# Kernel tuning notes

Measured on AMD Instinct MI355X. Metric: run time of the kernel, lower is better.

## Reference

```python
import jax, jax.numpy as jnp
import numpy as np

H = 9
N1, N2, N3 = 100000, 25000, 6250
E1, E2, E3 = 1200000, 300000, 75000
LAYERS = {"l1": (6, 32), "l2": (32, 64), "l3": (64, 128), "l4": (128, 128),
          "r1": (128, 64), "r2": (128, 64), "r3": (64, 32), "r4": (64, 32)}


def setup_inputs() -> dict:
    key = jax.random.key(0)
    ks = iter(jax.random.split(key, 64))
    d = {}
    d["x"] = jax.random.normal(next(ks), (N1, 6), jnp.float32)
    d["ei1"] = jax.random.randint(next(ks), (2, E1), 0, N1)
    d["ei2"] = jax.random.randint(next(ks), (2, E2), 0, N2)
    d["ei3"] = jax.random.randint(next(ks), (2, E3), 0, N3)
    d["clust2"] = jax.random.randint(next(ks), (N1,), 0, N2)
    d["clust3"] = jax.random.randint(next(ks), (N2,), 0, N3)
    for name, (cin, cout) in LAYERS.items():
        d[name + "_u"] = jax.random.normal(next(ks), (cin, H), jnp.float32) * 0.1
        d[name + "_c"] = jax.random.normal(next(ks), (H,), jnp.float32) * 0.1
        d[name + "_w"] = jax.random.normal(next(ks), (cin, H * cout), jnp.float32) * (1.0 / np.sqrt(cin))
        d[name + "_b"] = jnp.zeros((cout,), jnp.float32)
    d["fc1_w"] = jax.random.normal(next(ks), (32, 1024), jnp.float32) * (1.0 / np.sqrt(32))
    d["fc1_b"] = jnp.zeros((1024,), jnp.float32)
    d["fc2_w"] = jax.random.normal(next(ks), (1024, 3), jnp.float32) * (1.0 / np.sqrt(1024))
    d["fc2_b"] = jnp.zeros((3,), jnp.float32)
    return d


def _feast(x, ei, u, c, W, b):
    """FeaStConv (Verma et al., PyG semantics): per-edge head attention
    q = softmax(u^T (x_j - x_i) + c), mean aggregation, self-loops added."""
    n = x.shape[0]
    out = W.shape[1] // H
    loop = jnp.arange(n)
    src = jnp.concatenate([ei[0], loop])  # message source j
    dst = jnp.concatenate([ei[1], loop])  # message target i
    q = jax.nn.softmax((x[src] - x[dst]) @ u + c, axis=1)  # [E, H]
    msg = jnp.zeros((src.shape[0], out), x.dtype)
    for h in range(H):  # fixed head loop keeps peak memory at [E, out]
        msg = msg + q[:, h:h + 1] * (x @ W[:, h * out:(h + 1) * out])[src]
    agg = jax.ops.segment_sum(msg, dst, num_segments=n)
    cnt = jax.ops.segment_sum(jnp.ones((dst.shape[0],), x.dtype), dst, num_segments=n)
    return agg / cnt[:, None] + b  # cnt >= 1 thanks to self-loops


def _pool_mean(x, clust, n_out):
    s = jax.ops.segment_sum(x, clust, num_segments=n_out)
    c = jax.ops.segment_sum(jnp.ones((x.shape[0],), x.dtype), clust, num_segments=n_out)
    return s / jnp.maximum(c, 1.0)[:, None]


def _lrelu(v):
    return jax.nn.leaky_relu(v, 0.1)


def reference(x, ei1, ei2, ei3, clust2, clust3,
              l1_u, l1_c, l1_w, l1_b, l2_u, l2_c, l2_w, l2_b,
              l3_u, l3_c, l3_w, l3_b, l4_u, l4_c, l4_w, l4_b,
              r1_u, r1_c, r1_w, r1_b, r2_u, r2_c, r2_w, r2_b,
              r3_u, r3_c, r3_w, r3_b, r4_u, r4_c, r4_w, r4_b,
              fc1_w, fc1_b, fc2_w, fc2_b):
    x1 = _lrelu(_feast(x, ei1, l1_u, l1_c, l1_w, l1_b))           # [N1, 32]
    x2 = _pool_mean(x1, clust2, N2)                                # [N2, 32]
    x2 = _lrelu(_feast(x2, ei2, l2_u, l2_c, l2_w, l2_b))           # [N2, 64]
    x3 = _pool_mean(x2, clust3, N3)                                # [N3, 64]
    x3 = _lrelu(_feast(x3, ei3, l3_u, l3_c, l3_w, l3_b))           # [N3, 128]
    x3 = _lrelu(_feast(x3, ei3, l4_u, l4_c, l4_w, l4_b))           # [N3, 128]
    f2 = _feast(x3[clust3], ei2, r1_u, r1_c, r1_w, r1_b)           # unpool -> [N2, 64] (no act)
    x2 = jnp.concatenate([x2, f2], axis=1)                         # [N2, 128]
    x2 = _lrelu(_feast(x2, ei2, r2_u, r2_c, r2_w, r2_b))           # [N2, 64]
    f1 = _feast(x2[clust2], ei1, r3_u, r3_c, r3_w, r3_b)           # unpool -> [N1, 32] (no act)
    x1 = jnp.concatenate([x1, f1], axis=1)                         # [N1, 64]
    y = _lrelu(_feast(x1, ei1, r4_u, r4_c, r4_w, r4_b))            # [N1, 32]
    y = _lrelu(y @ fc1_w + fc1_b)                                  # [N1, 1024]
    y = y @ fc2_w + fc2_b                                          # [N1, 3]
    return y / jnp.maximum(jnp.linalg.norm(y, axis=1, keepdims=True), 1e-12)
```

## Files before the change

kernel.cpp:

```cpp
#include <hip/hip_runtime.h>
#include <cstddef>
#include <cstdint>

#define NH 9
#define QLD 16

typedef _Float16 f16x8 __attribute__((ext_vector_type(8)));
typedef _Float16 f16x4 __attribute__((ext_vector_type(4)));
typedef _Float16 f16x2 __attribute__((ext_vector_type(2)));
typedef float f32x4 __attribute__((ext_vector_type(4)));

static const int cN1 = 100000, cN2 = 25000, cN3 = 6250;
static const int cE1 = 1200000, cE2 = 300000, cE3 = 75000;

static inline unsigned ceil_div(size_t a, size_t b) { return (unsigned)((a + b - 1) / b); }

struct PackArgs {
    const float* W[8];
    const float* c[8];
    const float* u[8];
    int K[8], OUT[8], Kpad[8], base[8];
    int total;
};

__global__ void pack_b_all(PackArgs a, _Float16* __restrict__ wt)
{
    int i = blockIdx.x * 256 + threadIdx.x;
    if (i >= a.total) return;
    int li = 0;
#pragma unroll
    for (int j = 1; j < 8; ++j) li += (i >= a.base[j]);
    int r = i - a.base[li];
    int Kp = a.Kpad[li], K = a.K[li], OUT = a.OUT[li];
    int NC = NH * OUT, NCO = NC + OUT;
    int n = r / Kp, k = r % Kp;
    float v = 0.f;
    if (k < K) {
        if (n < NC) v = a.W[li][(size_t)k * NC + n];
        else if (n < NCO) {
            const float* cv = a.c[li];
            float t[NH], m = -1e30f;
#pragma unroll
            for (int h = 0; h < NH; ++h) { t[h] = cv[h]; m = fmaxf(m, t[h]); }
            float den = 0.f;
#pragma unroll
            for (int h = 0; h < NH; ++h) { t[h] = __expf(t[h] - m); den += t[h]; }
            int o = n - NC;
            float acc = 0.f;
#pragma unroll
            for (int h = 0; h < NH; ++h) acc += t[h] * a.W[li][(size_t)k * NC + h * OUT + o];
            v = acc / den;
        } else {
            v = a.u[li][(size_t)k * NH + (n - NCO)];
        }
    }
    wt[i] = (_Float16)v;
}

template <typename AT>
__global__ __launch_bounds__(256) void gemm_merged(
    const AT* __restrict__ A, int lda, const int* __restrict__ ridx,
    const _Float16* __restrict__ WT, int kpad,
    _Float16* __restrict__ C, _Float16* __restrict__ xuh,
    int M, int K, int NC, int OUT)
{
    const int N = NC + OUT + NH;
    const int NCO = NC + OUT;
    const int ldc = NCO + 16;
    const int BM = 64, BK = 32, LK = 40;
    __shared__ _Float16 As[BM][LK];
    __shared__ _Float16 Bs[64][LK];
    const int tid = threadIdx.x;
    const int row0 = blockIdx.y * BM, col0 = blockIdx.x * 64;
    const int lane = tid & 63, wv = tid >> 6;
    const int g = lane >> 4, r16 = lane & 15;
    const int wr = wv >> 1, wc = wv & 1;
    f32x4 acc[2][2] = {};
    for (int k0 = 0; k0 < K; k0 += BK) {
        if constexpr (sizeof(AT) == 2) {
            int r = tid >> 2, c0 = (tid & 3) * 8;
            int gr = row0 + r, gk = k0 + c0;
            f16x8 h = {};
            if (gr < M) {
                int ar = ridx ? ridx[gr] : gr;
                h = *(const f16x8*)((const _Float16*)A + (size_t)ar * lda + gk);
            }
            *(f16x8*)&As[r][c0] = h;
        } else {
            for (int l = tid; l < 512; l += 256) {
                int r = l >> 3, c0 = (l & 7) * 4;
                int gr = row0 + r, gk = k0 + c0;
                float v0 = 0.f, v1 = 0.f, v2 = 0.f, v3 = 0.f;
                if (gr < M) {
                    int ar = ridx ? ridx[gr] : gr;
                    const float* ap = (const float*)A + (size_t)ar * lda + gk;
                    if (gk < K)     v0 = ap[0];
                    if (gk + 1 < K) v1 = ap[1];
                    if (gk + 2 < K) v2 = ap[2];
                    if (gk + 3 < K) v3 = ap[3];
                }
                f16x4 h;
                h[0] = (_Float16)v0; h[1] = (_Float16)v1; h[2] = (_Float16)v2; h[3] = (_Float16)v3;
                *(f16x4*)&As[r][c0] = h;
            }
        }
        {
            int nn = tid >> 2, c0 = (tid & 3) * 8;
            int gn = col0 + nn, gk = k0 + c0;
            f16x8 h = {};
            if (gn < N) h = *(const f16x8*)(WT + (size_t)gn * kpad + gk);
            *(f16x8*)&Bs[nn][c0] = h;
        }
        __syncthreads();
        f16x8 af[2], bf[2];
#pragma unroll
        for (int i = 0; i < 2; ++i) af[i] = *(const f16x8*)&As[wr * 32 + i * 16 + r16][g * 8];
#pragma unroll
        for (int j = 0; j < 2; ++j) bf[j] = *(const f16x8*)&Bs[wc * 32 + j * 16 + r16][g * 8];
#pragma unroll
        for (int i = 0; i < 2; ++i)
#pragma unroll
            for (int j = 0; j < 2; ++j)
                acc[i][j] = __builtin_amdgcn_mfma_f32_16x16x32_f16(af[i], bf[j], acc[i][j], 0, 0, 0);
        __syncthreads();
    }
#pragma unroll
    for (int i = 0; i < 2; ++i)
#pragma unroll
        for (int j = 0; j < 2; ++j) {
            int gc = col0 + wc * 32 + j * 16 + r16;
            if (gc >= N) continue;
            int tcol = gc - NCO;
#pragma unroll
            for (int rr = 0; rr < 4; ++rr) {
                int gr = row0 + wr * 32 + i * 16 + g * 4 + rr;
                if (gr >= M) continue;
                _Float16 val = (_Float16)acc[i][j][rr];
                C[(size_t)gr * ldc + gc] = val;
                if (tcol >= 0) xuh[(size_t)gr * QLD + tcol] = val;
            }
        }
}

__global__ void count_idx(const int* __restrict__ idx, int n, int* __restrict__ cnt)
{
    int i = blockIdx.x * 256 + threadIdx.x;
    if (i < n) atomicAdd(&cnt[idx[i]], 1);
}

__global__ void count_both(const int* __restrict__ src, const int* __restrict__ dst, int E,
                           int* __restrict__ scnt, int* __restrict__ dcnt)
{
    int i = blockIdx.x * 256 + threadIdx.x;
    if (i >= E) return;
    atomicAdd(&scnt[src[i]], 1);
    atomicAdd(&dcnt[dst[i]], 1);
}

__global__ __launch_bounds__(1024) void scan1(const int* __restrict__ in, int* __restrict__ out,
                                              int* __restrict__ part, int n)
{
    __shared__ int wsum[16];
    const int tid = threadIdx.x, lane = tid & 63, wv = tid >> 6;
    int i = blockIdx.x * 1024 + tid;
    int v = (i < n) ? in[i] : 0;
    int acc = v;
#pragma unroll
    for (int off = 1; off < 64; off <<= 1) {
        int t = __shfl_up(acc, off);
        if (lane >= off) acc += t;
    }
    if (lane == 63) wsum[wv] = acc;
    __syncthreads();
    if (wv == 0 && lane < 16) {
        int s = wsum[lane];
        int a2 = s;
#pragma unroll
        for (int off = 1; off < 16; off <<= 1) {
            int t = __shfl_up(a2, off);
            if (lane >= off) a2 += t;
        }
        wsum[lane] = a2 - s;
    }
    __syncthreads();
    int ex = wsum[wv] + acc - v;
    if (i < n) out[i] = ex;
    if (part && tid == 1023) part[blockIdx.x] = ex + v;
}

__global__ void scan_add(int* __restrict__ out, const int* __restrict__ part, int n)
{
    int i = blockIdx.x * 1024 + threadIdx.x;
    if (i < n) out[i] += part[blockIdx.x];
}

__global__ void fill_src(const int* __restrict__ soffB, const int* __restrict__ scnt,
                         int* __restrict__ srcs, int n, int ebias)
{
    int i = blockIdx.x * 256 + threadIdx.x;
    if (i >= n) return;
    int b = soffB[i] - ebias, c = scnt[i];
    for (int k = 0; k < c; ++k) srcs[b + k] = i;
}

__global__ void scatter_dst(const int* __restrict__ src, const int* __restrict__ dst, int E,
                            const int* __restrict__ soffB, int* __restrict__ curs,
                            int* __restrict__ dsts, int ebias)
{
    int e = blockIdx.x * 256 + threadIdx.x;
    if (e >= E) return;
    int s = src[e];
    int ps = soffB[s] - ebias + atomicAdd(&curs[s], 1);
    dsts[ps] = dst[e];
}

template <int OUT>
__global__ __launch_bounds__(256) void feast_msg(
    const int* __restrict__ srcs, const int* __restrict__ dsts, int E,
    const _Float16* __restrict__ xwa, const _Float16* __restrict__ xuh,
    const float* __restrict__ cvec, const int* __restrict__ ds,
    int* __restrict__ curd, _Float16* __restrict__ msg)
{
    constexpr int NC = NH * OUT, NCO = NC + OUT, LDR = NCO + 16;
    const int T = OUT / 32;
    size_t tid = (size_t)blockIdx.x * 256 + threadIdx.x;
    int e = (int)(tid / T);
    int ch = (int)(tid % T);
    if (e >= E) return;
    int s = srcs[e], d = dsts[e];
    int beg = ds[d];
    int deg = ds[d + 1] - beg;
    int pd;
    if (T == 1) {
        pd = beg + (atomicAdd(&curd[d], 1) % deg);
    } else {
        int lane = threadIdx.x & 63;
        int pv = 0;
        if (ch == 0) pv = beg + (atomicAdd(&curd[d], 1) % deg);
        pd = __shfl(pv, (lane / T) * T);
    }
    f16x8 u8s = *(const f16x8*)(xwa + (size_t)s * LDR + NCO);
    f16x2 u2s = *(const f16x2*)(xwa + (size_t)s * LDR + NCO + 8);
    f16x8 u8d = *(const f16x8*)(xuh + (size_t)d * QLD);
    f16x2 u2d = *(const f16x2*)(xuh + (size_t)d * QLD + 8);
    float t[NH];
    float m = -1e30f;
#pragma unroll
    for (int h = 0; h < 8; ++h) {
        t[h] = (float)u8s[h] - (float)u8d[h] + cvec[h];
        m = fmaxf(m, t[h]);
    }
    t[8] = (float)u2s[0] - (float)u2d[0] + cvec[8];
    m = fmaxf(m, t[8]);
    float den = 0.f;
#pragma unroll
    for (int h = 0; h < NH; ++h) { t[h] = __expf(t[h] - m); den += t[h]; }
    float sc = 1.f / (den * (float)(deg + 1));

    const f16x8* xrow = (const f16x8*)(xwa + (size_t)s * LDR);
    float acc[32] = {};
#pragma unroll
    for (int h = 0; h < NH; ++h) {
        float qh = t[h] * sc;
        const f16x8* xh = xrow + h * (OUT / 8) + ch * 4;
#pragma unroll
        for (int v = 0; v < 4; ++v) {
            f16x8 x8 = xh[v];
#pragma unroll
            for (int j = 0; j < 8; ++j) acc[v * 8 + j] += qh * (float)x8[j];
        }
    }
    f16x8* mo = (f16x8*)(msg + (size_t)pd * OUT + ch * 32);
#pragma unroll
    for (int v = 0; v < 4; ++v) {
        f16x8 r;
#pragma unroll
        for (int j = 0; j < 8; ++j) r[j] = (_Float16)acc[v * 8 + j];
        mo[v] = r;
    }
}

template <int OUT>
__global__ __launch_bounds__(256) void feast_red(
    const int* __restrict__ ds,
    const _Float16* __restrict__ msg, const _Float16* __restrict__ xwa,
    const float* __restrict__ bias, _Float16* __restrict__ outp,
    int n, int ldo, int col0, int act,
    const int* __restrict__ clust, float* __restrict__ pooled)
{
    constexpr int NC = NH * OUT, LDR = NC + OUT + 16;
    const int L = OUT / 8;
    size_t tid = (size_t)blockIdx.x * 256 + threadIdx.x;
    int d = (int)(tid / L);
    int p = (int)(tid % L);
    if (d >= n) return;
    int beg = ds[d];
    int end = ds[d + 1];
    int deg = end - beg;
    float acc[8] = {};
    int i = beg;
    for (; i + 2 <= end; i += 2) {
        f16x8 v0 = *(const f16x8*)(msg + (size_t)i * OUT + p * 8);
        f16x8 v1 = *(const f16x8*)(msg + (size_t)(i + 1) * OUT + p * 8);
#pragma unroll
        for (int j = 0; j < 8; ++j) acc[j] += (float)v0[j] + (float)v1[j];
    }
    if (i < end) {
        f16x8 v0 = *(const f16x8*)(msg + (size_t)i * OUT + p * 8);
#pragma unroll
        for (int j = 0; j < 8; ++j) acc[j] += (float)v0[j];
    }
    float sc = 1.f / (float)(deg + 1);
    f16x8 sv = *(const f16x8*)(xwa + (size_t)d * LDR + NC + p * 8);
    float o[8];
    f16x8 oh;
#pragma unroll
    for (int j = 0; j < 8; ++j) {
        float v = acc[j] + (float)sv[j] * sc + bias[p * 8 + j];
        if (act) v = v > 0.f ? v : 0.1f * v;
        o[j] = v;
        oh[j] = (_Float16)v;
    }
    *(f16x8*)(outp + (size_t)d * ldo + col0 + p * 8) = oh;
    if (clust) {
        float* pp = pooled + (size_t)clust[d] * OUT + p * 8;
#pragma unroll
        for (int j = 0; j < 8; ++j) unsafeAtomicAdd(&pp[j], o[j]);
    }
}

__global__ void pool_div(float* __restrict__ pooled, const int* __restrict__ pcnt, int C, int m)
{
    size_t tid = (size_t)blockIdx.x * 256 + threadIdx.x;
    int j = (int)(tid / C);
    if (j >= m) return;
    pooled[tid] /= fmaxf((float)pcnt[j], 1.f);
}

__global__ void w1_to_f16t(const float* __restrict__ w1, _Float16* __restrict__ w1t)
{
    int i = blockIdx.x * 256 + threadIdx.x;
    if (i >= 32 * 1024) return;
    int n = i >> 5, k = i & 31;
    w1t[i] = (_Float16)w1[k * 1024 + n];
}

__global__ __launch_bounds__(256) void fc_head2(
    const _Float16* __restrict__ yin, const _Float16* __restrict__ w1t,
    const float* __restrict__ b1, const float* __restrict__ w2,
    const float* __restrict__ b2, float* __restrict__ outp, int n)
{
    const int lane = threadIdx.x & 63, wv = threadIdx.x >> 6;
    const int g = lane >> 4, r16 = lane & 15;
    const int node0 = blockIdx.x * 64 + wv * 16;

    f16x8 afrag = {};
    int anode = node0 + r16;
    if (anode < n) afrag = *(const f16x8*)(yin + (size_t)anode * 32 + g * 8);

    float o0[4] = {0.f, 0.f, 0.f, 0.f};
    float o1[4] = {0.f, 0.f, 0.f, 0.f};
    float o2[4] = {0.f, 0.f, 0.f, 0.f};
    const f32x4 zero4 = {0.f, 0.f, 0.f, 0.f};

#pragma unroll 2
    for (int t = 0; t < 64; ++t) {
        const f16x8 bfrag = *(const f16x8*)(w1t + ((size_t)(t * 16 + r16)) * 32 + g * 8);
        f32x4 d = __builtin_amdgcn_mfma_f32_16x16x32_f16(afrag, bfrag, zero4, 0, 0, 0);
        int kh = t * 16 + r16;
        float b1v = b1[kh];
        float w20 = w2[kh * 3], w21 = w2[kh * 3 + 1], w22 = w2[kh * 3 + 2];
#pragma unroll
        for (int r = 0; r < 4; ++r) {
            float h = d[r] + b1v;
            h = h > 0.f ? h : 0.1f * h;
            o0[r] += h * w20;
            o1[r] += h * w21;
            o2[r] += h * w22;
        }
    }
#pragma unroll
    for (int r = 0; r < 4; ++r) {
#pragma unroll
        for (int off = 1; off < 16; off <<= 1) {
            o0[r] += __shfl_xor(o0[r], off);
            o1[r] += __shfl_xor(o1[r], off);
            o2[r] += __shfl_xor(o2[r], off);
        }
    }
    if (r16 == 0) {
#pragma unroll
        for (int r = 0; r < 4; ++r) {
            int node = node0 + g * 4 + r;
            if (node >= n) continue;
            float v0 = o0[r] + b2[0];
            float v1 = o1[r] + b2[1];
            float v2 = o2[r] + b2[2];
            float nr = fmaxf(sqrtf(v0 * v0 + v1 * v1 + v2 * v2), 1e-12f);
            outp[(size_t)node * 3 + 0] = v0 / nr;
            outp[(size_t)node * 3 + 1] = v1 / nr;
            outp[(size_t)node * 3 + 2] = v2 / nr;
        }
    }
}

static void launch_msg(int outC, const int* srcs, const int* dsts, int E,
                       const _Float16* xwa, const _Float16* xuh, const float* cvec,
                       const int* ds, int* curd, _Float16* msg, hipStream_t stream)
{
    dim3 g(ceil_div((size_t)E * (outC / 32), 256));
    if (outC == 32)       feast_msg<32><<<g, 256, 0, stream>>>(srcs, dsts, E, xwa, xuh, cvec, ds, curd, msg);
    else if (outC == 64)  feast_msg<64><<<g, 256, 0, stream>>>(srcs, dsts, E, xwa, xuh, cvec, ds, curd, msg);
    else                  feast_msg<128><<<g, 256, 0, stream>>>(srcs, dsts, E, xwa, xuh, cvec, ds, curd, msg);
}

static void launch_red(int outC, const int* ds,
                       const _Float16* msg, const _Float16* xwa, const float* bias,
                       _Float16* outp, int n, int ldo, int col0, int act,
                       const int* clust, float* pooled, hipStream_t stream)
{
    dim3 g(ceil_div((size_t)n * (outC / 8), 256));
    if (outC == 32)       feast_red<32><<<g, 256, 0, stream>>>(ds, msg, xwa, bias, outp, n, ldo, col0, act, clust, pooled);
    else if (outC == 64)  feast_red<64><<<g, 256, 0, stream>>>(ds, msg, xwa, bias, outp, n, ldo, col0, act, clust, pooled);
    else                  feast_red<128><<<g, 256, 0, stream>>>(ds, msg, xwa, bias, outp, n, ldo, col0, act, clust, pooled);
}

extern "C" void kernel_launch(void* const* d_in, const int* in_sizes, int n_in,
                              void* d_out, int out_size, void* d_ws, size_t ws_size,
                              hipStream_t stream)
{
    const float* x      = (const float*)d_in[0];
    const int*   ei1    = (const int*)d_in[1];
    const int*   ei2    = (const int*)d_in[2];
    const int*   ei3    = (const int*)d_in[3];
    const int*   clust2 = (const int*)d_in[4];
    const int*   clust3 = (const int*)d_in[5];
    const float* lp[8][4];
    for (int i = 0; i < 8; ++i)
        for (int j = 0; j < 4; ++j)
            lp[i][j] = (const float*)d_in[6 + i * 4 + j];
    const float* fc1_w = (const float*)d_in[38];
    const float* fc1_b = (const float*)d_in[39];
    const float* fc2_w = (const float*)d_in[40];
    const float* fc2_b = (const float*)d_in[41];
    float* out = (float*)d_out;

    static const int lK[8]   = {6, 32, 64, 128, 128, 128, 64, 64};
    static const int lOUT[8] = {32, 64, 128, 128, 64, 64, 32, 32};

    char* ws = (char*)d_ws;
    size_t off = 0;
    auto alloc = [&](size_t b) { size_t p = off; off += (b + 255) & ~(size_t)255; return p; };
    _Float16* XWA = (_Float16*)(ws + alloc((size_t)cN1 * 336 * 2));
    _Float16* MSG = (_Float16*)(ws + alloc((size_t)cE1 * 32 * 2));
    _Float16* XUH = (_Float16*)(ws + alloc((size_t)cN1 * QLD * 2));
    _Float16* X1CAT = (_Float16*)(ws + alloc((size_t)cN1 * 64 * 2));
    _Float16* X2CAT = (_Float16*)(ws + alloc((size_t)cN2 * 128 * 2));
    _Float16* X2B   = (_Float16*)(ws + alloc((size_t)cN2 * 64 * 2));
    _Float16* X3    = (_Float16*)(ws + alloc((size_t)cN3 * 128 * 2));
    _Float16* YB    = (_Float16*)(ws + alloc((size_t)cN1 * 32 * 2));
    float* GATH = (float*)(ws + alloc((size_t)cN2 * 32 * 4));
    float* P3   = (float*)(ws + alloc((size_t)cN3 * 64 * 4));
    int* SRCS1 = (int*)(ws + alloc((size_t)cE1 * 4));
    int* SRCS2 = (int*)(ws + alloc((size_t)cE2 * 4));
    int* SRCS3 = (int*)(ws + alloc((size_t)cE3 * 4));
    int* DSTS1 = (int*)(ws + alloc((size_t)cE1 * 4));
    int* DSTS2 = (int*)(ws + alloc((size_t)cE2 * 4));
    int* DSTS3 = (int*)(ws + alloc((size_t)cE3 * 4));
    int* DS1 = (int*)(ws + alloc((size_t)2 * cN1 * 4));
    int* DS2 = (int*)(ws + alloc((size_t)2 * cN2 * 4));
    int* DS3 = (int*)(ws + alloc((size_t)2 * cN3 * 4));
    size_t zn = (size_t)4 * (cN1 + cN2 + cN3) + cN2 + cN3;
    int* ZBLK = (int*)(ws + alloc(zn * 4));
    int* CB1 = ZBLK;
    int* CURS1 = CB1 + 2 * cN1;
    int* CURD1 = CURS1 + cN1;
    int* CB2 = CURD1 + cN1;
    int* CURS2 = CB2 + 2 * cN2;
    int* CURD2 = CURS2 + cN2;
    int* CB3 = CURD2 + cN2;
    int* CURS3 = CB3 + 2 * cN3;
    int* CURD3 = CURS3 + cN3;
    int* PC2 = CURD3 + cN3;
    int* PC3 = PC2 + cN2;
    int* PART = (int*)(ws + alloc(1024 * 4));
    _Float16* W1T = (_Float16*)(ws + alloc((size_t)32 * 1024 * 2));
    PackArgs pa;
    int ptot = 0;
    for (int i = 0; i < 8; ++i) {
        pa.W[i] = lp[i][2]; pa.c[i] = lp[i][1]; pa.u[i] = lp[i][0];
        pa.K[i] = lK[i]; pa.OUT[i] = lOUT[i];
        pa.Kpad[i] = (lK[i] + 31) & ~31;
        pa.base[i] = ptot;
        ptot += (NH * lOUT[i] + lOUT[i] + NH) * pa.Kpad[i];
    }
    pa.total = ptot;
    _Float16* WT = (_Float16*)(ws + alloc((size_t)ptot * 2));

    auto run_scan = [&](const int* in, int* outp, int n) {
        int nb = (n + 1023) / 1024;
        scan1<<<nb, 1024, 0, stream>>>(in, outp, nb > 1 ? PART : nullptr, n);
        if (nb > 1) {
            scan1<<<1, 1024, 0, stream>>>(PART, PART, nullptr, nb);
            scan_add<<<nb, 1024, 0, stream>>>(outp, PART, n);
        }
    };

    hipMemsetAsync(ZBLK, 0, zn * 4, stream);

    auto build = [&](const int* ei, int E, int n, int* cb, int* curs, int* ds,
                     int* srcs, int* dsts) {
        count_both<<<ceil_div(E, 256), 256, 0, stream>>>(ei, ei + E, E, cb + n, cb);
        run_scan(cb, ds, 2 * n);
        fill_src<<<ceil_div(n, 256), 256, 0, stream>>>(ds + n, cb + n, srcs, n, E);
        scatter_dst<<<ceil_div(E, 256), 256, 0, stream>>>(ei, ei + E, E, ds + n, curs, dsts, E);
    };
    build(ei1, cE1, cN1, CB1, CURS1, DS1, SRCS1, DSTS1);
    build(ei2, cE2, cN2, CB2, CURS2, DS2, SRCS2, DSTS2);
    build(ei3, cE3, cN3, CB3, CURS3, DS3, SRCS3, DSTS3);

    pack_b_all<<<ceil_div(ptot, 256), 256, 0, stream>>>(pa, WT);
    w1_to_f16t<<<ceil_div(32 * 1024, 256), 256, 0, stream>>>(fc1_w, W1T);

    auto feast = [&](auto* xin, int ldx, const int* ridx, int n, int cin, int li,
                     const int* srcs, const int* dsts, const int* ds, int* curd, int E,
                     _Float16* dstp, int ldo, int col0, int act,
                     const int* pclust, float* pooled) {
        int outC = lOUT[li];
        int NC = NH * outC;
        int N = NC + outC + NH;
        gemm_merged<<<dim3(ceil_div(N, 64), ceil_div(n, 64)), 256, 0, stream>>>(
            xin, ldx, ridx, WT + (size_t)pa.base[li], pa.Kpad[li], XWA, XUH, n, cin, NC, outC);
        launch_msg(outC, srcs, dsts, E, XWA, XUH, lp[li][1], ds, curd, MSG, stream);
        launch_red(outC, ds, MSG, XWA, lp[li][3], dstp, n, ldo, col0, act, pclust, pooled, stream);
    };

    hipMemsetAsync(GATH, 0, (size_t)cN2 * 32 * 4, stream);
    count_idx<<<ceil_div(cN1, 256), 256, 0, stream>>>(clust2, cN1, PC2);
    feast(x, 6, nullptr, cN1, 6, 0, SRCS1, DSTS1, DS1, CURD1, cE1, X1CAT, 64, 0, 1, clust2, GATH);
    pool_div<<<ceil_div((size_t)cN2 * 32, 256), 256, 0, stream>>>(GATH, PC2, 32, cN2);

    count_idx<<<ceil_div(cN2, 256), 256, 0, stream>>>(clust3, cN2, PC3);
    hipMemsetAsync(P3, 0, (size_t)cN3 * 64 * 4, stream);
    feast(GATH, 32, nullptr, cN2, 32, 1, SRCS2, DSTS2, DS2, CURD2, cE2, X2CAT, 128, 0, 1, clust3, P3);
    pool_div<<<ceil_div((size_t)cN3 * 64, 256), 256, 0, stream>>>(P3, PC3, 64, cN3);

    feast(P3, 64, nullptr, cN3, 64, 2, SRCS3, DSTS3, DS3, CURD3, cE3, X3, 128, 0, 1, nullptr, nullptr);
    feast(X3, 128, nullptr, cN3, 128, 3, SRCS3, DSTS3, DS3, CURD3, cE3, X3, 128, 0, 1, nullptr, nullptr);

    feast(X3, 128, clust3, cN2, 128, 4, SRCS2, DSTS2, DS2, CURD2, cE2, X2CAT, 128, 64, 0, nullptr, nullptr);

    feast(X2CAT, 128, nullptr, cN2, 128, 5, SRCS2, DSTS2, DS2, CURD2, cE2, X2B, 64, 0, 1, nullptr, nullptr);

    feast(X2B, 64, clust2, cN1, 64, 6, SRCS1, DSTS1, DS1, CURD1, cE1, X1CAT, 64, 32, 0, nullptr, nullptr);

    feast(X1CAT, 64, nullptr, cN1, 64, 7, SRCS1, DSTS1, DS1, CURD1, cE1, YB, 32, 0, 1, nullptr, nullptr);

    fc_head2<<<ceil_div(cN1, 64), 256, 0, stream>>>(YB, W1T, fc1_b, fc2_w, fc2_b, out, cN1);

    (void)in_sizes; (void)n_in; (void)out_size; (void)ws_size;
}
```

Baseline: 1.108 ms.

## Precompute per-edge destination slots once at graph build instead of per layer

Destination slot assignment for each edge is computed once during graph construction and stored with the destination id as an int2 record. The per-layer message kernels no longer do an atomic on a destination cursor, the degree lookup, or the modulo, and the mean scale moves into the reduction kernel. The reduction loop is also unrolled to four messages per iteration. The trade-off is a larger 8-byte edge record per edge and extra atomics in the one-time build kernel.

```diff
diff --git a/kernel.cpp b/kernel.cpp
--- a/kernel.cpp
+++ b/kernel.cpp
@@ -203,23 +203,24 @@
     for (int k = 0; k < c; ++k) srcs[b + k] = i;
 }
 
-__global__ void scatter_dst(const int* __restrict__ src, const int* __restrict__ dst, int E,
-                            const int* __restrict__ soffB, int* __restrict__ curs,
-                            int* __restrict__ dsts, int ebias)
+__global__ void scatter_light(const int* __restrict__ src, const int* __restrict__ dst, int E,
+                              const int* __restrict__ soffB, int* __restrict__ curs,
+                              const int* __restrict__ doff, int* __restrict__ curd,
+                              int2* __restrict__ erec, int ebias)
 {
     int e = blockIdx.x * 256 + threadIdx.x;
     if (e >= E) return;
-    int s = src[e];
+    int s = src[e], d = dst[e];
     int ps = soffB[s] - ebias + atomicAdd(&curs[s], 1);
-    dsts[ps] = dst[e];
+    int pd = doff[d] + atomicAdd(&curd[d], 1);
+    erec[ps] = make_int2(d, pd);
 }
 
 template <int OUT>
 __global__ __launch_bounds__(256) void feast_msg(
-    const int* __restrict__ srcs, const int* __restrict__ dsts, int E,
+    const int* __restrict__ srcs, const int2* __restrict__ erec, int E,
     const _Float16* __restrict__ xwa, const _Float16* __restrict__ xuh,
-    const float* __restrict__ cvec, const int* __restrict__ ds,
-    int* __restrict__ curd, _Float16* __restrict__ msg)
+    const float* __restrict__ cvec, _Float16* __restrict__ msg)
 {
     constexpr int NC = NH * OUT, NCO = NC + OUT, LDR = NCO + 16;
     const int T = OUT / 32;
@@ -227,18 +228,9 @@
     int e = (int)(tid / T);
     int ch = (int)(tid % T);
     if (e >= E) return;
-    int s = srcs[e], d = dsts[e];
-    int beg = ds[d];
-    int deg = ds[d + 1] - beg;
-    int pd;
-    if (T == 1) {
-        pd = beg + (atomicAdd(&curd[d], 1) % deg);
-    } else {
-        int lane = threadIdx.x & 63;
-        int pv = 0;
-        if (ch == 0) pv = beg + (atomicAdd(&curd[d], 1) % deg);
-        pd = __shfl(pv, (lane / T) * T);
-    }
+    int s = srcs[e];
+    int2 ed = erec[e];
+    int d = ed.x, pd = ed.y;
     f16x8 u8s = *(const f16x8*)(xwa + (size_t)s * LDR + NCO);
     f16x2 u2s = *(const f16x2*)(xwa + (size_t)s * LDR + NCO + 8);
     f16x8 u8d = *(const f16x8*)(xuh + (size_t)d * QLD);
@@ -255,7 +247,7 @@
     float den = 0.f;
 #pragma unroll
     for (int h = 0; h < NH; ++h) { t[h] = __expf(t[h] - m); den += t[h]; }
-    float sc = 1.f / (den * (float)(deg + 1));
+    float sc = 1.f / den;
 
     const f16x8* xrow = (const f16x8*)(xwa + (size_t)s * LDR);
     float acc[32] = {};
@@ -299,13 +291,16 @@
     int deg = end - beg;
     float acc[8] = {};
     int i = beg;
-    for (; i + 2 <= end; i += 2) {
+    for (; i + 4 <= end; i += 4) {
         f16x8 v0 = *(const f16x8*)(msg + (size_t)i * OUT + p * 8);
         f16x8 v1 = *(const f16x8*)(msg + (size_t)(i + 1) * OUT + p * 8);
-#pragma unroll
-        for (int j = 0; j < 8; ++j) acc[j] += (float)v0[j] + (float)v1[j];
-    }
-    if (i < end) {
+        f16x8 v2 = *(const f16x8*)(msg + (size_t)(i + 2) * OUT + p * 8);
+        f16x8 v3 = *(const f16x8*)(msg + (size_t)(i + 3) * OUT + p * 8);
+#pragma unroll
+        for (int j = 0; j < 8; ++j)
+            acc[j] += ((float)v0[j] + (float)v1[j]) + ((float)v2[j] + (float)v3[j]);
+    }
+    for (; i < end; ++i) {
         f16x8 v0 = *(const f16x8*)(msg + (size_t)i * OUT + p * 8);
 #pragma unroll
         for (int j = 0; j < 8; ++j) acc[j] += (float)v0[j];
@@ -316,7 +311,7 @@
     f16x8 oh;
 #pragma unroll
     for (int j = 0; j < 8; ++j) {
-        float v = acc[j] + (float)sv[j] * sc + bias[p * 8 + j];
+        float v = (acc[j] + (float)sv[j]) * sc + bias[p * 8 + j];
         if (act) v = v > 0.f ? v : 0.1f * v;
         o[j] = v;
         oh[j] = (_Float16)v;
@@ -404,14 +399,14 @@
     }
 }
 
-static void launch_msg(int outC, const int* srcs, const int* dsts, int E,
+static void launch_msg(int outC, const int* srcs, const int2* erec, int E,
                        const _Float16* xwa, const _Float16* xuh, const float* cvec,
-                       const int* ds, int* curd, _Float16* msg, hipStream_t stream)
+                       _Float16* msg, hipStream_t stream)
 {
     dim3 g(ceil_div((size_t)E * (outC / 32), 256));
-    if (outC == 32)       feast_msg<32><<<g, 256, 0, stream>>>(srcs, dsts, E, xwa, xuh, cvec, ds, curd, msg);
-    else if (outC == 64)  feast_msg<64><<<g, 256, 0, stream>>>(srcs, dsts, E, xwa, xuh, cvec, ds, curd, msg);
-    else                  feast_msg<128><<<g, 256, 0, stream>>>(srcs, dsts, E, xwa, xuh, cvec, ds, curd, msg);
+    if (outC == 32)       feast_msg<32><<<g, 256, 0, stream>>>(srcs, erec, E, xwa, xuh, cvec, msg);
+    else if (outC == 64)  feast_msg<64><<<g, 256, 0, stream>>>(srcs, erec, E, xwa, xuh, cvec, msg);
+    else                  feast_msg<128><<<g, 256, 0, stream>>>(srcs, erec, E, xwa, xuh, cvec, msg);
 }
 
 static void launch_red(int outC, const int* ds,
@@ -464,9 +459,9 @@
     int* SRCS1 = (int*)(ws + alloc((size_t)cE1 * 4));
     int* SRCS2 = (int*)(ws + alloc((size_t)cE2 * 4));
     int* SRCS3 = (int*)(ws + alloc((size_t)cE3 * 4));
-    int* DSTS1 = (int*)(ws + alloc((size_t)cE1 * 4));
-    int* DSTS2 = (int*)(ws + alloc((size_t)cE2 * 4));
-    int* DSTS3 = (int*)(ws + alloc((size_t)cE3 * 4));
+    int2* EREC1 = (int2*)(ws + alloc((size_t)cE1 * 8));
+    int2* EREC2 = (int2*)(ws + alloc((size_t)cE2 * 8));
+    int2* EREC3 = (int2*)(ws + alloc((size_t)cE3 * 8));
     int* DS1 = (int*)(ws + alloc((size_t)2 * cN1 * 4));
     int* DS2 = (int*)(ws + alloc((size_t)2 * cN2 * 4));
     int* DS3 = (int*)(ws + alloc((size_t)2 * cN3 * 4));
@@ -508,22 +503,22 @@
 
     hipMemsetAsync(ZBLK, 0, zn * 4, stream);
 
-    auto build = [&](const int* ei, int E, int n, int* cb, int* curs, int* ds,
-                     int* srcs, int* dsts) {
+    auto build = [&](const int* ei, int E, int n, int* cb, int* curs, int* curd, int* ds,
+                     int* srcs, int2* erec) {
         count_both<<<ceil_div(E, 256), 256, 0, stream>>>(ei, ei + E, E, cb + n, cb);
         run_scan(cb, ds, 2 * n);
         fill_src<<<ceil_div(n, 256), 256, 0, stream>>>(ds + n, cb + n, srcs, n, E);
-        scatter_dst<<<ceil_div(E, 256), 256, 0, stream>>>(ei, ei + E, E, ds + n, curs, dsts, E);
+        scatter_light<<<ceil_div(E, 256), 256, 0, stream>>>(ei, ei + E, E, ds + n, curs, ds, curd, erec, E);
     };
-    build(ei1, cE1, cN1, CB1, CURS1, DS1, SRCS1, DSTS1);
-    build(ei2, cE2, cN2, CB2, CURS2, DS2, SRCS2, DSTS2);
-    build(ei3, cE3, cN3, CB3, CURS3, DS3, SRCS3, DSTS3);
+    build(ei1, cE1, cN1, CB1, CURS1, CURD1, DS1, SRCS1, EREC1);
+    build(ei2, cE2, cN2, CB2, CURS2, CURD2, DS2, SRCS2, EREC2);
+    build(ei3, cE3, cN3, CB3, CURS3, CURD3, DS3, SRCS3, EREC3);
 
     pack_b_all<<<ceil_div(ptot, 256), 256, 0, stream>>>(pa, WT);
     w1_to_f16t<<<ceil_div(32 * 1024, 256), 256, 0, stream>>>(fc1_w, W1T);
 
     auto feast = [&](auto* xin, int ldx, const int* ridx, int n, int cin, int li,
-                     const int* srcs, const int* dsts, const int* ds, int* curd, int E,
+                     const int* srcs, const int2* erec, const int* ds, int E,
                      _Float16* dstp, int ldo, int col0, int act,
                      const int* pclust, float* pooled) {
         int outC = lOUT[li];
@@ -531,30 +526,30 @@
         int N = NC + outC + NH;
         gemm_merged<<<dim3(ceil_div(N, 64), ceil_div(n, 64)), 256, 0, stream>>>(
             xin, ldx, ridx, WT + (size_t)pa.base[li], pa.Kpad[li], XWA, XUH, n, cin, NC, outC);
-        launch_msg(outC, srcs, dsts, E, XWA, XUH, lp[li][1], ds, curd, MSG, stream);
+        launch_msg(outC, srcs, erec, E, XWA, XUH, lp[li][1], MSG, stream);
         launch_red(outC, ds, MSG, XWA, lp[li][3], dstp, n, ldo, col0, act, pclust, pooled, stream);
     };
 
     hipMemsetAsync(GATH, 0, (size_t)cN2 * 32 * 4, stream);
     count_idx<<<ceil_div(cN1, 256), 256, 0, stream>>>(clust2, cN1, PC2);
-    feast(x, 6, nullptr, cN1, 6, 0, SRCS1, DSTS1, DS1, CURD1, cE1, X1CAT, 64, 0, 1, clust2, GATH);
+    feast(x, 6, nullptr, cN1, 6, 0, SRCS1, EREC1, DS1, cE1, X1CAT, 64, 0, 1, clust2, GATH);
     pool_div<<<ceil_div((size_t)cN2 * 32, 256), 256, 0, stream>>>(GATH, PC2, 32, cN2);
 
     count_idx<<<ceil_div(cN2, 256), 256, 0, stream>>>(clust3, cN2, PC3);
     hipMemsetAsync(P3, 0, (size_t)cN3 * 64 * 4, stream);
-    feast(GATH, 32, nullptr, cN2, 32, 1, SRCS2, DSTS2, DS2, CURD2, cE2, X2CAT, 128, 0, 1, clust3, P3);
+    feast(GATH, 32, nullptr, cN2, 32, 1, SRCS2, EREC2, DS2, cE2, X2CAT, 128, 0, 1, clust3, P3);
     pool_div<<<ceil_div((size_t)cN3 * 64, 256), 256, 0, stream>>>(P3, PC3, 64, cN3);
 
-    feast(P3, 64, nullptr, cN3, 64, 2, SRCS3, DSTS3, DS3, CURD3, cE3, X3, 128, 0, 1, nullptr, nullptr);
-    feast(X3, 128, nullptr, cN3, 128, 3, SRCS3, DSTS3, DS3, CURD3, cE3, X3, 128, 0, 1, nullptr, nullptr);
-
-    feast(X3, 128, clust3, cN2, 128, 4, SRCS2, DSTS2, DS2, CURD2, cE2, X2CAT, 128, 64, 0, nullptr, nullptr);
-
-    feast(X2CAT, 128, nullptr, cN2, 128, 5, SRCS2, DSTS2, DS2, CURD2, cE2, X2B, 64, 0, 1, nullptr, nullptr);
-
-    feast(X2B, 64, clust2, cN1, 64, 6, SRCS1, DSTS1, DS1, CURD1, cE1, X1CAT, 64, 32, 0, nullptr, nullptr);
-
-    feast(X1CAT, 64, nullptr, cN1, 64, 7, SRCS1, DSTS1, DS1, CURD1, cE1, YB, 32, 0, 1, nullptr, nullptr);
+    feast(P3, 64, nullptr, cN3, 64, 2, SRCS3, EREC3, DS3, cE3, X3, 128, 0, 1, nullptr, nullptr);
+    feast(X3, 128, nullptr, cN3, 128, 3, SRCS3, EREC3, DS3, cE3, X3, 128, 0, 1, nullptr, nullptr);
+
+    feast(X3, 128, clust3, cN2, 128, 4, SRCS2, EREC2, DS2, cE2, X2CAT, 128, 64, 0, nullptr, nullptr);
+
+    feast(X2CAT, 128, nullptr, cN2, 128, 5, SRCS2, EREC2, DS2, cE2, X2B, 64, 0, 1, nullptr, nullptr);
+
+    feast(X2B, 64, clust2, cN1, 64, 6, SRCS1, EREC1, DS1, cE1, X1CAT, 64, 32, 0, nullptr, nullptr);
+
+    feast(X1CAT, 64, nullptr, cN1, 64, 7, SRCS1, EREC1, DS1, cE1, YB, 32, 0, 1, nullptr, nullptr);
 
     fc_head2<<<ceil_div(cN1, 64), 256, 0, stream>>>(YB, W1T, fc1_b, fc2_w, fc2_b, out, cN1);
 
```

After: 1.068 ms. 3.6% less time.
